# Kernel optimization log

Measured on AMD Instinct MI355X. Metric: run time of the kernel, lower is better.

The kernel has to match this reference:

```python
import jax, jax.numpy as jnp
import numpy as np
from jax import lax

B, T, V, E, H, M = 512, 60, 50000, 300, 512, 256


def _lstm_final_h(x_emb, seqlen, kernel, bias):
    """BasicLSTMCell (gate order i,j,f,o; forget_bias=1.0) with dynamic_rnn
    sequence_length semantics: state stops updating at t >= seqlen.
    x_emb: [B, T, E]; returns final h: [B, H]."""
    b = x_emb.shape[0]
    h0 = jnp.zeros((b, H), x_emb.dtype)
    c0 = jnp.zeros((b, H), x_emb.dtype)

    def step(carry, inp):
        c, h = carry
        xt, t = inp
        z = jnp.concatenate([xt, h], axis=1) @ kernel + bias  # [B, 4H]
        i, j, f, o = jnp.split(z, 4, axis=1)
        nc = c * jax.nn.sigmoid(f + 1.0) + jax.nn.sigmoid(i) * jnp.tanh(j)
        nh = jnp.tanh(nc) * jax.nn.sigmoid(o)
        valid = (t < seqlen)[:, None]
        return (jnp.where(valid, nc, c), jnp.where(valid, nh, h)), None

    (c, h), _ = lax.scan(step, (c0, h0),
                         (jnp.swapaxes(x_emb, 0, 1), jnp.arange(T)))
    return h


def setup_inputs() -> dict:
    key = jax.random.key(0)
    ks = jax.random.split(key, 8)
    return {
        "input1": jax.random.randint(ks[0], (B, T), 0, V, dtype=jnp.int32),
        "input2": jax.random.randint(ks[1], (B, T), 0, V, dtype=jnp.int32),
        "seqlen1": jax.random.randint(ks[2], (B,), 1, T + 1, dtype=jnp.int32),
        "seqlen2": jax.random.randint(ks[3], (B,), 1, T + 1, dtype=jnp.int32),
        "embeddings": jax.random.normal(ks[4], (V, E), jnp.float32) * 0.1,
        "lstm_kernel": jax.random.normal(ks[5], (E + H, 4 * H), jnp.float32) * 0.02,
        "lstm_bias": jnp.zeros((4 * H,), jnp.float32),
        "W1": jax.random.normal(ks[6], (4 * (H + 1) + 1, M), jnp.float32) * 0.02,
        "b1": jnp.zeros((1, M), jnp.float32),
        "W2": jax.random.normal(ks[7], (M, 2), jnp.float32) * 0.02,
        "b2": jnp.zeros((1, 2), jnp.float32),
    }


def reference(input1, input2, seqlen1, seqlen2, embeddings,
              lstm_kernel, lstm_bias, W1, b1, W2, b2):
    x1 = embeddings[input1]  # [B, T, E]
    x2 = embeddings[input2]
    h1 = _lstm_final_h(x1, seqlen1, lstm_kernel, lstm_bias)  # [B, H]
    h2 = _lstm_final_h(x2, seqlen2, lstm_kernel, lstm_bias)
    len1 = (seqlen1.astype(jnp.float32) / float(T))[:, None]
    len2 = (seqlen2.astype(jnp.float32) / float(T))[:, None]
    h1 = jnp.concatenate([h1, len1], axis=1)  # [B, H+1]
    h2 = jnp.concatenate([h2, len2], axis=1)
    h_sub = h1 - h2
    h_dist = jnp.sum(h_sub * h_sub, axis=1, keepdims=True)  # [B, 1]
    h_mul = h1 * h2
    h_combined = jnp.concatenate([h1, h2, h_sub, h_dist, h_mul], axis=1)
    e1 = jax.nn.relu(h_combined @ W1 + b1)  # dropout keep_prob=1 -> identity
    preds = e1 @ W2 + b2  # [B, 2]
    return preds
```

## Files before the change

### kernel.cpp

```cpp
#include <hip/hip_runtime.h>
#include <hip/hip_bf16.h>

#define BATCH 512
#define TT 60
#define EDIM 300
#define HDIM 512
#define KP1 2112
#define MDIM 256
#define V48 2400000

typedef __bf16 bf16x4 __attribute__((ext_vector_type(4)));
typedef __bf16 bf16x8 __attribute__((ext_vector_type(8)));
typedef float  f32x16 __attribute__((ext_vector_type(16)));

#define GLL16(g, l) __builtin_amdgcn_global_load_lds( \
    (const __attribute__((address_space(1))) void*)(g), \
    (__attribute__((address_space(3))) void*)(l), 16, 0, 0)

__device__ __forceinline__ float sigm(float x) {
    return 1.0f / (1.0f + __expf(-x));
}
__device__ __forceinline__ float tanh_fast(float x) {
    float e = __expf(-2.0f * fabsf(x));
    float r = (1.0f - e) / (1.0f + e);
    return x >= 0.0f ? r : -r;
}


__global__ __launch_bounds__(256) void sort_rows(const int* __restrict__ sl1,
                                                 const int* __restrict__ sl2,
                                                 int* __restrict__ rowinfo,
                                                 unsigned* __restrict__ step_done) {
    __shared__ unsigned cnt[61];
    __shared__ unsigned off[61];
    int tid = threadIdx.x;
    if (tid < 61) cnt[tid] = 0;
    if (tid >= 64 && tid < 80) step_done[tid - 64] = 0;
    __syncthreads();
    for (int i = tid; i < 1024; i += 256) {
        int sl = (i < 512) ? sl1[i] : sl2[i - 512];
        atomicAdd(&cnt[60 - sl], 1u);
    }
    __syncthreads();
    if (tid == 0) {
        unsigned s = 0;
        for (int k = 0; k < 61; ++k) { off[k] = s; s += cnt[k]; }
    }
    __syncthreads();
    for (int i = tid; i < 1024; i += 256) {
        int sc = i >= 512;
        int b = i & 511;
        int sl = sc ? sl2[b] : sl1[b];
        unsigned pos = atomicAdd(&off[60 - sl], 1u);
        rowinfo[pos] = b | (sc << 15) | (sl << 20);
    }
}

__global__ __launch_bounds__(256) void prep_w(const float* __restrict__ kern,
                                              __bf16* __restrict__ wf) {
    __shared__ float tile[64][65];
    int bk = blockIdx.x % 14;
    int bn = blockIdx.x / 14;
    int k0 = bk * 64, n0 = bn * 64;
    int tid = threadIdx.x;
#pragma unroll
    for (int i = 0; i < 16; ++i) {
        int id = i * 256 + tid;
        int kk = id >> 6, nn = id & 63;
        int kg = k0 + kk;
        int src = (kg < 300) ? kg : (kg >= 384 ? kg - 84 : -1);
        tile[kk][nn] = (src >= 0) ? kern[(size_t)src * 2048 + n0 + nn] : 0.0f;
    }
    __syncthreads();
    int gate = n0 >> 9;
    int nt = gate >> 1;
#pragma unroll
    for (int i = 0; i < 2; ++i) {
        int id = i * 256 + tid;
        int nn = id >> 3, k8 = id & 7;
        bf16x8 hv, lv;
#pragma unroll
        for (int j = 0; j < 8; ++j) {
            float v = tile[k8 * 8 + j][nn];
            __bf16 h = (__bf16)v;
            hv[j] = h;
            lv[j] = (__bf16)(v - (float)h);
        }
        int cg = (((n0 & 511) >> 4) + (nn >> 4));
        int hc = nn & 15;
        int lzc = ((gate & 1) << 4) + hc;
        int kglob = k0 + k8 * 8;
        int c = kglob >> 7;
        int j = (kglob >> 4) & 7;
        int half = k8 & 1;
        size_t o = (size_t)cg * 114688 + c * 16384 + (j * 4 + nt * 2) * 512
                 + (half * 32 + lzc) * 8;
        *(bf16x8*)(wf + o) = hv;
        *(bf16x8*)(wf + o + 512) = lv;
    }
}

__global__ __launch_bounds__(256) void prep_w1(const float* __restrict__ W1,
                                               __bf16* __restrict__ w1h,
                                               __bf16* __restrict__ w1l) {
    __shared__ float tile[64][65];
    int bk = blockIdx.x % 33;
    int bn = blockIdx.x / 33;
    int k0 = bk * 64, n0 = bn * 64;
    int tid = threadIdx.x;
#pragma unroll
    for (int i = 0; i < 16; ++i) {
        int id = i * 256 + tid;
        int kk = id >> 6, nn = id & 63;
        int kg = k0 + kk;
        tile[kk][nn] = (kg < 2053) ? W1[(size_t)kg * MDIM + n0 + nn] : 0.0f;
    }
    __syncthreads();
#pragma unroll
    for (int i = 0; i < 2; ++i) {
        int id = i * 256 + tid;
        int nn = id >> 3, k8 = (id & 7) * 8;
        bf16x8 hv, lv;
#pragma unroll
        for (int j = 0; j < 8; ++j) {
            float v = tile[k8 + j][nn];
            __bf16 h = (__bf16)v;
            hv[j] = h;
            lv[j] = (__bf16)(v - (float)h);
        }
        size_t o = (size_t)(n0 + nn) * KP1 + k0 + k8;
        *(bf16x8*)(w1h + o) = hv;
        *(bf16x8*)(w1l + o) = lv;
    }
}

__global__ __launch_bounds__(256) void prep_emb(const float* __restrict__ emb,
                                                __bf16* __restrict__ embB) {
    int id = blockIdx.x * 256 + threadIdx.x;
    if (id >= V48) return;
    int tok = id / 48;
    int k8 = id - tok * 48;
    int k0 = k8 * 8;
    float vv[8];
    const float* er = emb + (size_t)tok * EDIM + k0;
    if (k0 + 8 <= EDIM) {
        float4 f0 = *(const float4*)er;
        float4 f1 = *(const float4*)(er + 4);
        vv[0] = f0.x; vv[1] = f0.y; vv[2] = f0.z; vv[3] = f0.w;
        vv[4] = f1.x; vv[5] = f1.y; vv[6] = f1.z; vv[7] = f1.w;
    } else if (k0 < EDIM) {
        float4 f0 = *(const float4*)er;
        vv[0] = f0.x; vv[1] = f0.y; vv[2] = f0.z; vv[3] = f0.w;
        vv[4] = vv[5] = vv[6] = vv[7] = 0.f;
    } else {
#pragma unroll
        for (int j = 0; j < 8; ++j) vv[j] = 0.f;
    }
    bf16x8 hv, lv;
#pragma unroll
    for (int j = 0; j < 8; ++j) {
        __bf16 h = (__bf16)vv[j];
        hv[j] = h;
        lv[j] = (__bf16)(vv[j] - (float)h);
    }
    size_t o = (size_t)tok * 768 + k0;
    *(bf16x8*)(embB + o) = hv;
    *(bf16x8*)(embB + o + 384) = lv;
}

#define ZSTR 72

__global__ __launch_bounds__(256, 2) void lstm_all(
    const int* __restrict__ in1, const int* __restrict__ in2,
    const int* __restrict__ rowinfo,
    const __bf16* __restrict__ embB, const float* __restrict__ bias,
    const __bf16* __restrict__ wf,
    __bf16* __restrict__ XfH,
    unsigned* __restrict__ step_done,
    float* __restrict__ h_state) {

    int bx = blockIdx.x;
    int xcd = bx & 7;
    int loc = bx >> 3;
    int u = loc >> 3;
    int p = xcd & 1;
    int bt = (u < 4) ? ((u << 1) | p) : (15 - (((u - 4) << 1) | p));
    int cg = ((xcd >> 1) << 3) | (loc & 7);

    __shared__ __align__(16) __bf16 Bb[2][16384];
    __shared__ int info_s[64];

    int tid = threadIdx.x;
    int w = tid >> 6, lane = tid & 63, l31 = lane & 31;
    int s = w >> 1, kg = w & 1;

    if (tid < 64) info_s[tid] = rowinfo[bt * 64 + tid];
    __syncthreads();
    int t_end = info_s[0] >> 20;

    int rowl = s * 32 + l31;
    int inf_r = info_s[rowl];
    const int* tokptr = ((((inf_r >> 15) & 1) ? in2 : in1)) + (inf_r & 511) * TT;

    int hc16 = tid & 15;
    int hcol = (cg << 4) + hc16;
    float bi = bias[hcol], bj = bias[512 + hcol];
    float bfv = bias[1024 + hcol], bo = bias[1536 + hcol];

    float c_reg[4] = {0.f, 0.f, 0.f, 0.f};
    float h_reg[4] = {0.f, 0.f, 0.f, 0.f};

    const __bf16* wb = wf + (size_t)cg * 114688;
    auto stageB = [&](int c, int buf) {
        const __bf16* src = wb + c * 16384 + w * 4096 + lane * 8;
        __bf16* dst = &Bb[buf][w * 4096 + lane * 8];
#pragma unroll
        for (int i = 0; i < 8; ++i)
            GLL16(src + i * 512, dst + i * 512);
    };

    int ew = kg * 64 + ((lane >> 5) << 3);
    size_t hw_off = (size_t)((s * 2 + kg) * 4) * 4096 + lane * 8;

    for (int t = 0; t < t_end; ++t) {
        f32x16 acc[2];
#pragma unroll
        for (int nt = 0; nt < 2; ++nt)
#pragma unroll
            for (int r = 0; r < 16; ++r) acc[nt][r] = 0.0f;

        int tok = tokptr[t];
        const __bf16* eb = embB + (size_t)tok * 768 + ew;
        const __bf16* hrd = XfH + ((size_t)t * 16 + bt) * 65536 + hw_off;

        bf16x8 aH[4], aL[4];
        stageB(0, 0);
#pragma unroll
        for (int jj = 0; jj < 4; ++jj) {
            aH[jj] = *(const bf16x8*)(eb + jj * 16);
            aL[jj] = *(const bf16x8*)(eb + 384 + jj * 16);
        }

        if (t > 0 && tid == 0) {
            unsigned target = 32u * (unsigned)t;
            int guard = 0;
            while (__hip_atomic_load(step_done + bt, __ATOMIC_RELAXED,
                                     __HIP_MEMORY_SCOPE_AGENT) < target) {
                __builtin_amdgcn_s_sleep(2);
                if (++guard > (1 << 20)) break;
            }
        }
        __syncthreads();

#pragma unroll
        for (int c = 0; c < 7; ++c) {
            int cur = c & 1;
            bf16x8 nH[4], nL[4];
            if (c < 6) {
                stageB(c + 1, 1 - cur);
                if (c < 2) {
                    const __bf16* en = eb + (c + 1) * 128;
#pragma unroll
                    for (int jj = 0; jj < 4; ++jj) {
                        nH[jj] = *(const bf16x8*)(en + jj * 16);
                        nL[jj] = *(const bf16x8*)(en + 384 + jj * 16);
                    }
                } else {
                    const __bf16* An = hrd + (c - 2) * 4096;
#pragma unroll
                    for (int jj = 0; jj < 4; ++jj) {
                        nH[jj] = *(const bf16x8*)(An + jj * 1024);
                        nL[jj] = *(const bf16x8*)(An + jj * 1024 + 512);
                    }
                }
            }
#pragma unroll
            for (int jj = 0; jj < 4; ++jj) {
                int j = kg * 4 + jj;
#pragma unroll
                for (int nt = 0; nt < 2; ++nt) {
                    int T0 = (j * 4 + nt * 2) * 512 + lane * 8;
                    bf16x8 bh = *(const bf16x8*)(&Bb[cur][T0]);
                    bf16x8 bl = *(const bf16x8*)(&Bb[cur][T0 + 512]);
                    acc[nt] = __builtin_amdgcn_mfma_f32_32x32x16_bf16(aH[jj], bh, acc[nt], 0, 0, 0);
                    acc[nt] = __builtin_amdgcn_mfma_f32_32x32x16_bf16(aH[jj], bl, acc[nt], 0, 0, 0);
                    acc[nt] = __builtin_amdgcn_mfma_f32_32x32x16_bf16(aL[jj], bh, acc[nt], 0, 0, 0);
                }
            }
            if (c < 6) {
#pragma unroll
                for (int jj = 0; jj < 4; ++jj) { aH[jj] = nH[jj]; aL[jj] = nL[jj]; }
            }
            __syncthreads();
        }

        float* zs = (float*)&Bb[1][0];
        if (kg == 0) {
#pragma unroll
            for (int nt = 0; nt < 2; ++nt)
#pragma unroll
                for (int r = 0; r < 16; ++r) {
                    int rl = s * 32 + (r & 3) + ((r >> 2) << 3) + ((lane >> 5) << 2);
                    zs[rl * ZSTR + nt * 32 + l31] = acc[nt][r];
                }
        }
        __syncthreads();
        if (kg == 1) {
#pragma unroll
            for (int nt = 0; nt < 2; ++nt)
#pragma unroll
                for (int r = 0; r < 16; ++r) {
                    int rl = s * 32 + (r & 3) + ((r >> 2) << 3) + ((lane >> 5) << 2);
                    zs[rl * ZSTR + nt * 32 + l31] += acc[nt][r];
                }
        }
        __syncthreads();

        __bf16* zh = &Bb[0][0];
#pragma unroll
        for (int i = 0; i < 4; ++i) {
            int rl = i * 16 + (tid >> 4);
            int info = info_s[rl];
            int sl = info >> 20;
            float zi = zs[rl * ZSTR + hc16]      + bi;
            float zj = zs[rl * ZSTR + 16 + hc16] + bj;
            float zf = zs[rl * ZSTR + 32 + hc16] + bfv;
            float zo = zs[rl * ZSTR + 48 + hc16] + bo;
            float c_old = c_reg[i];
            float h_old = h_reg[i];
            float nc = c_old * sigm(zf + 1.0f) + sigm(zi) * tanh_fast(zj);
            float nh = tanh_fast(nc) * sigm(zo);
            bool valid = t < sl;
            float cs = valid ? nc : c_old;
            float hs = valid ? nh : h_old;
            c_reg[i] = cs;
            h_reg[i] = hs;
            __bf16 hh = (__bf16)hs;
            int grp = hc16 >> 3, e = hc16 & 7;
            zh[(grp * 64 + rl) * 8 + e] = hh;
            zh[((2 + grp) * 64 + rl) * 8 + e] = (__bf16)(hs - (float)hh);
        }
        __syncthreads();

        if (t + 1 < t_end) {
            int plane = tid >> 7;
            int grp = (tid >> 6) & 1;
            int rl = tid & 63;
            ulonglong2 uv = *(const ulonglong2*)(zh + ((plane * 2 + grp) * 64 + rl) * 8);
            int s2 = rl >> 5;
            size_t base = ((size_t)(t + 1) * 16 + bt) * 65536
                        + (size_t)((s2 * 2 + ((cg >> 2) & 1)) * 4 + (cg >> 3)) * 4096
                        + (cg & 3) * 1024 + plane * 512 + (grp * 32 + (rl & 31)) * 8;
            unsigned long long* dst = (unsigned long long*)(XfH + base);
            __hip_atomic_store(dst,     uv.x, __ATOMIC_RELAXED, __HIP_MEMORY_SCOPE_AGENT);
            __hip_atomic_store(dst + 1, uv.y, __ATOMIC_RELAXED, __HIP_MEMORY_SCOPE_AGENT);
        }
        __syncthreads();
        if (t + 1 < t_end && tid == 0)
            __hip_atomic_fetch_add(step_done + bt, 1u, __ATOMIC_RELAXED,
                                   __HIP_MEMORY_SCOPE_AGENT);
    }

#pragma unroll
    for (int i = 0; i < 4; ++i) {
        int rl = i * 16 + (tid >> 4);
        int info = info_s[rl];
        int b = info & 511, sc = (info >> 15) & 1;
        h_state[(size_t)((sc << 9) + b) * HDIM + hcol] = h_reg[i];
    }
}

__global__ __launch_bounds__(256) void head1(const float* __restrict__ h_state,
                                             const int* __restrict__ sl1,
                                             const int* __restrict__ sl2,
                                             __bf16* __restrict__ hch,
                                             __bf16* __restrict__ hcl) {
    int b = blockIdx.x;
    int tid = threadIdx.x;
    const float* h1 = h_state + (size_t)b * HDIM;
    const float* h2 = h_state + (size_t)(512 + b) * HDIM;
    size_t ro = (size_t)b * KP1;
    float l1 = (float)sl1[b] / (float)TT;
    float l2 = (float)sl2[b] / (float)TT;
    float part = 0.0f;
#pragma unroll
    for (int i = 0; i < 2; ++i) {
        int k = i * 256 + tid;
        float a = h1[k], c = h2[k];
        float sv = a - c;
        float mv = a * c;
        __bf16 xh;
        xh = (__bf16)a;  hch[ro + k] = xh;         hcl[ro + k] = (__bf16)(a - (float)xh);
        xh = (__bf16)c;  hch[ro + 513 + k] = xh;   hcl[ro + 513 + k] = (__bf16)(c - (float)xh);
        xh = (__bf16)sv; hch[ro + 1026 + k] = xh;  hcl[ro + 1026 + k] = (__bf16)(sv - (float)xh);
        xh = (__bf16)mv; hch[ro + 1540 + k] = xh;  hcl[ro + 1540 + k] = (__bf16)(mv - (float)xh);
        part += sv * sv;
    }
    __shared__ float red[4];
#pragma unroll
    for (int off = 32; off > 0; off >>= 1) part += __shfl_down(part, off, 64);
    if ((tid & 63) == 0) red[tid >> 6] = part;
    __syncthreads();
    if (tid == 0) {
        float d = red[0] + red[1] + red[2] + red[3];
        float ls = l1 - l2;
        d += ls * ls;
        float vals[5] = {l1, l2, ls, d, l1 * l2};
        int pos[5] = {512, 1025, 1538, 1539, 2052};
#pragma unroll
        for (int i = 0; i < 5; ++i) {
            __bf16 xh = (__bf16)vals[i];
            hch[ro + pos[i]] = xh;
            hcl[ro + pos[i]] = (__bf16)(vals[i] - (float)xh);
        }
    }
}

__global__ __launch_bounds__(512, 2) void head2m(
    const __bf16* __restrict__ hch, const __bf16* __restrict__ hcl,
    const __bf16* __restrict__ w1h, const __bf16* __restrict__ w1l,
    float* __restrict__ part) {

    __shared__ __align__(16) __bf16 Bb[2][64 * 512];

    int tid = threadIdx.x;
    int bx = blockIdx.x;
    int mt = bx >> 3;
    int n2 = (bx >> 2) & 1;
    int ks = bx & 3;
    int w = tid >> 6, lane = tid & 63, l31 = lane & 31;
    int half8 = (lane >> 5) << 3;
    int s = w >> 1, nh = w & 1;
    int kbase = ks * 528;

    int k8 = tid & 15;
    int jb = k8 >> 1;
    int rb = (tid >> 4) & 31;
    size_t gboff[8];
    int lo[8];
#pragma unroll
    for (int i = 0; i < 8; ++i) {
        int r = ((i & 3) << 5) + rb;
        int plane = i >> 2;
        int ng = n2 * 128 + r;
        gboff[i] = (size_t)ng * KP1 + k8 * 8;
        int nt = r >> 5;
        int colp = ((r & 31) + (jb << 2)) & 31;
        lo[i] = ((((jb << 2) + nt) << 1) + plane) * 512 + (colp + ((k8 & 1) << 5)) * 8;
    }

    const __bf16* Ah0 = hch + (size_t)(mt * 128 + s * 32 + l31) * KP1 + kbase + half8;
    const __bf16* Al0 = hcl + (size_t)(mt * 128 + s * 32 + l31) * KP1 + kbase + half8;

    bf16x8 rB[8];
    f32x16 acc[2];
#pragma unroll
    for (int nt = 0; nt < 2; ++nt)
#pragma unroll
        for (int r = 0; r < 16; ++r) acc[nt][r] = 0.0f;

#pragma unroll
    for (int i = 0; i < 8; ++i)
        rB[i] = *(const bf16x8*)(((i >= 4) ? w1l : w1h) + gboff[i] + kbase);
#pragma unroll
    for (int i = 0; i < 8; ++i) *(bf16x8*)(&Bb[0][lo[i]]) = rB[i];
    __syncthreads();

    for (int c = 0; c < 5; ++c) {
        int cur = c & 1;
        if (c < 4) {
            int k0 = kbase + (c + 1) * 128;
            bool tail = (c + 1 == 4);
#pragma unroll
            for (int i = 0; i < 8; ++i) {
                if (!tail || k8 < 2)
                    rB[i] = *(const bf16x8*)(((i >= 4) ? w1l : w1h) + gboff[i] + k0);
            }
        }
        int jmax = (c == 4) ? 1 : 8;
        for (int j = 0; j < jmax; ++j) {
            bf16x8 ah = *(const bf16x8*)(Ah0 + c * 128 + j * 16);
            bf16x8 al = *(const bf16x8*)(Al0 + c * 128 + j * 16);
            int cp = ((l31 + (j << 2)) & 31) + ((lane >> 5) << 5);
#pragma unroll
            for (int ntl = 0; ntl < 2; ++ntl) {
                int ntg = nh * 2 + ntl;
                const __bf16* bp = &Bb[cur][(((j << 2) + ntg) << 1) * 512 + cp * 8];
                bf16x8 bh = *(const bf16x8*)bp;
                bf16x8 bl = *(const bf16x8*)(bp + 512);
                acc[ntl] = __builtin_amdgcn_mfma_f32_32x32x16_bf16(ah, bh, acc[ntl], 0, 0, 0);
                acc[ntl] = __builtin_amdgcn_mfma_f32_32x32x16_bf16(ah, bl, acc[ntl], 0, 0, 0);
                acc[ntl] = __builtin_amdgcn_mfma_f32_32x32x16_bf16(al, bh, acc[ntl], 0, 0, 0);
            }
        }
        if (c < 4) {
#pragma unroll
            for (int i = 0; i < 8; ++i) *(bf16x8*)(&Bb[1 - cur][lo[i]]) = rB[i];
        }
        __syncthreads();
    }

#pragma unroll
    for (int ntl = 0; ntl < 2; ++ntl)
#pragma unroll
        for (int r = 0; r < 16; ++r) {
            int row = mt * 128 + s * 32 + (r & 3) + ((r >> 2) << 3) + ((lane >> 5) << 2);
            int col = n2 * 128 + nh * 64 + ntl * 32 + l31;
            part[((size_t)ks * 512 + row) * MDIM + col] = acc[ntl][r];
        }
}

__global__ __launch_bounds__(256) void head3(const float* __restrict__ part,
                                             const float* __restrict__ b1,
                                             const float* __restrict__ W2,
                                             const float* __restrict__ b2,
                                             float* __restrict__ out) {
    int row = blockIdx.x;
    int tid = threadIdx.x;
    float sv = b1[tid];
#pragma unroll
    for (int ks = 0; ks < 4; ++ks)
        sv += part[((size_t)ks * 512 + row) * MDIM + tid];
    float e = fmaxf(sv, 0.0f);
    float p0 = e * W2[tid * 2 + 0];
    float p1 = e * W2[tid * 2 + 1];
#pragma unroll
    for (int off = 32; off > 0; off >>= 1) {
        p0 += __shfl_down(p0, off, 64);
        p1 += __shfl_down(p1, off, 64);
    }
    __shared__ float r0[4], r1[4];
    if ((tid & 63) == 0) { r0[tid >> 6] = p0; r1[tid >> 6] = p1; }
    __syncthreads();
    if (tid == 0) out[row * 2 + 0] = r0[0] + r0[1] + r0[2] + r0[3] + b2[0];
    if (tid == 1) out[row * 2 + 1] = r1[0] + r1[1] + r1[2] + r1[3] + b2[1];
}

extern "C" void kernel_launch(void* const* d_in, const int* in_sizes, int n_in,
                              void* d_out, int out_size, void* d_ws, size_t ws_size,
                              hipStream_t stream) {
    const int*   in1  = (const int*)d_in[0];
    const int*   in2  = (const int*)d_in[1];
    const int*   sl1  = (const int*)d_in[2];
    const int*   sl2  = (const int*)d_in[3];
    const float* emb  = (const float*)d_in[4];
    const float* kern = (const float*)d_in[5];
    const float* bias = (const float*)d_in[6];
    const float* W1   = (const float*)d_in[7];
    const float* b1   = (const float*)d_in[8];
    const float* W2   = (const float*)d_in[9];
    const float* b2   = (const float*)d_in[10];
    float* out = (float*)d_out;

    char* ws = (char*)d_ws;
    int*      rowinfo   = (int*)ws;
    unsigned* step_done = (unsigned*)(ws + 4096u);
    float*  h_state = (float*)(ws + 2097152u);
    __bf16* wf   = (__bf16*)(ws + 6291456u);
    __bf16* hch  = (__bf16*)(ws + 13631488u);
    __bf16* hcl  = (__bf16*)(ws + 15794176u);
    __bf16* w1h  = (__bf16*)(ws + 17956864u);
    __bf16* w1l  = (__bf16*)(ws + 19038208u);
    float*  part = (float*)(ws + 20119552u);
    __bf16* embB = (__bf16*)(ws + 23068672u);
    __bf16* XfH  = (__bf16*)(ws + 100663296u);

    hipMemsetAsync(ws + 13631488u, 0, 4325376u, stream);
    hipMemsetAsync(ws + 100663296u, 0, 2097152u, stream);

    sort_rows<<<dim3(1), dim3(256), 0, stream>>>(sl1, sl2, rowinfo, step_done);
    prep_w<<<dim3(14 * 32), dim3(256), 0, stream>>>(kern, wf);
    prep_w1<<<dim3(33 * 4), dim3(256), 0, stream>>>(W1, w1h, w1l);
    prep_emb<<<dim3(9375), dim3(256), 0, stream>>>(emb, embB);

    lstm_all<<<dim3(512), dim3(256), 0, stream>>>(
        in1, in2, rowinfo, embB, bias, wf, XfH, step_done, h_state);

    head1<<<dim3(512), dim3(256), 0, stream>>>(h_state, sl1, sl2, hch, hcl);
    head2m<<<dim3(32), dim3(512), 0, stream>>>(hch, hcl, w1h, w1l, part);
    head3<<<dim3(512), dim3(256), 0, stream>>>(part, b1, W2, b2, out);
}
```

Measured before the change: 1.273 ms.

## Load LSTM weight fragments directly into registers and defer step barrier

Replaces the double-buffered LDS staging of weight tiles (global_load_lds plus a per-chunk __syncthreads) with direct global-to-register loads of each wave's B fragments. The cross-block step wait moves to chunk 2, so the embedding-input chunks run before the dependency on the previous step's h. The two k-group partial sums go to separate LDS buffers and are added during the gate computation, which removes one barrier and one read-modify-write pass. The aim is fewer barriers and less LDS traffic per timestep. In exchange it adds register pressure and relies on global/L2 latency for the weights with no LDS staging.

Result: slower. 2.102 ms (+65.1%).

```diff
diff --git a/kernel.cpp b/kernel.cpp
--- a/kernel.cpp
+++ b/kernel.cpp
@@ -12,10 +12,6 @@
 typedef __bf16 bf16x4 __attribute__((ext_vector_type(4)));
 typedef __bf16 bf16x8 __attribute__((ext_vector_type(8)));
 typedef float  f32x16 __attribute__((ext_vector_type(16)));
-
-#define GLL16(g, l) __builtin_amdgcn_global_load_lds( \
-    (const __attribute__((address_space(1))) void*)(g), \
-    (__attribute__((address_space(3))) void*)(l), 16, 0, 0)
 
 __device__ __forceinline__ float sigm(float x) {
     return 1.0f / (1.0f + __expf(-x));
@@ -168,7 +164,7 @@
     *(bf16x8*)(embB + o + 384) = lv;
 }
 
-#define ZSTR 72
+#define ZSTR 68
 
 __global__ __launch_bounds__(256, 2) void lstm_all(
     const int* __restrict__ in1, const int* __restrict__ in2,
@@ -187,7 +183,8 @@
     int bt = (u < 4) ? ((u << 1) | p) : (15 - (((u - 4) << 1) | p));
     int cg = ((xcd >> 1) << 3) | (loc & 7);
 
-    __shared__ __align__(16) __bf16 Bb[2][16384];
+    __shared__ float zs[2][64 * ZSTR];
+    __shared__ __align__(16) __bf16 zh[2 * 2 * 64 * 8];
     __shared__ int info_s[64];
 
     int tid = threadIdx.x;
@@ -210,14 +207,7 @@
     float c_reg[4] = {0.f, 0.f, 0.f, 0.f};
     float h_reg[4] = {0.f, 0.f, 0.f, 0.f};
 
-    const __bf16* wb = wf + (size_t)cg * 114688;
-    auto stageB = [&](int c, int buf) {
-        const __bf16* src = wb + c * 16384 + w * 4096 + lane * 8;
-        __bf16* dst = &Bb[buf][w * 4096 + lane * 8];
-#pragma unroll
-        for (int i = 0; i < 8; ++i)
-            GLL16(src + i * 512, dst + i * 512);
-    };
+    const __bf16* wbl = wf + (size_t)cg * 114688 + (size_t)kg * 8192 + lane * 8;
 
     int ew = kg * 64 + ((lane >> 5) << 3);
     size_t hw_off = (size_t)((s * 2 + kg) * 4) * 4096 + lane * 8;
@@ -234,30 +224,39 @@
         const __bf16* hrd = XfH + ((size_t)t * 16 + bt) * 65536 + hw_off;
 
         bf16x8 aH[4], aL[4];
-        stageB(0, 0);
 #pragma unroll
         for (int jj = 0; jj < 4; ++jj) {
             aH[jj] = *(const bf16x8*)(eb + jj * 16);
             aL[jj] = *(const bf16x8*)(eb + 384 + jj * 16);
         }
 
-        if (t > 0 && tid == 0) {
-            unsigned target = 32u * (unsigned)t;
-            int guard = 0;
-            while (__hip_atomic_load(step_done + bt, __ATOMIC_RELAXED,
-                                     __HIP_MEMORY_SCOPE_AGENT) < target) {
-                __builtin_amdgcn_s_sleep(2);
-                if (++guard > (1 << 20)) break;
+#pragma unroll
+        for (int c = 0; c < 7; ++c) {
+            const __bf16* bc = wbl + c * 16384;
+            bf16x8 bH[4][2], bL[4][2];
+#pragma unroll
+            for (int jj = 0; jj < 4; ++jj)
+#pragma unroll
+                for (int nt = 0; nt < 2; ++nt) {
+                    bH[jj][nt] = *(const bf16x8*)(bc + jj * 2048 + nt * 1024);
+                    bL[jj][nt] = *(const bf16x8*)(bc + jj * 2048 + nt * 1024 + 512);
+                }
+
+            if (c == 2 && t > 0) {
+                if (tid == 0) {
+                    unsigned target = 32u * (unsigned)t;
+                    int guard = 0;
+                    while (__hip_atomic_load(step_done + bt, __ATOMIC_RELAXED,
+                                             __HIP_MEMORY_SCOPE_AGENT) < target) {
+                        __builtin_amdgcn_s_sleep(1);
+                        if (++guard > (1 << 20)) break;
+                    }
+                }
+                __syncthreads();
             }
-        }
-        __syncthreads();
-
-#pragma unroll
-        for (int c = 0; c < 7; ++c) {
-            int cur = c & 1;
+
             bf16x8 nH[4], nL[4];
             if (c < 6) {
-                stageB(c + 1, 1 - cur);
                 if (c < 2) {
                     const __bf16* en = eb + (c + 1) * 128;
 #pragma unroll
@@ -274,58 +273,39 @@
                     }
                 }
             }
-#pragma unroll
-            for (int jj = 0; jj < 4; ++jj) {
-                int j = kg * 4 + jj;
+
+#pragma unroll
+            for (int jj = 0; jj < 4; ++jj)
 #pragma unroll
                 for (int nt = 0; nt < 2; ++nt) {
-                    int T0 = (j * 4 + nt * 2) * 512 + lane * 8;
-                    bf16x8 bh = *(const bf16x8*)(&Bb[cur][T0]);
-                    bf16x8 bl = *(const bf16x8*)(&Bb[cur][T0 + 512]);
-                    acc[nt] = __builtin_amdgcn_mfma_f32_32x32x16_bf16(aH[jj], bh, acc[nt], 0, 0, 0);
-                    acc[nt] = __builtin_amdgcn_mfma_f32_32x32x16_bf16(aH[jj], bl, acc[nt], 0, 0, 0);
-                    acc[nt] = __builtin_amdgcn_mfma_f32_32x32x16_bf16(aL[jj], bh, acc[nt], 0, 0, 0);
+                    acc[nt] = __builtin_amdgcn_mfma_f32_32x32x16_bf16(aH[jj], bH[jj][nt], acc[nt], 0, 0, 0);
+                    acc[nt] = __builtin_amdgcn_mfma_f32_32x32x16_bf16(aH[jj], bL[jj][nt], acc[nt], 0, 0, 0);
+                    acc[nt] = __builtin_amdgcn_mfma_f32_32x32x16_bf16(aL[jj], bH[jj][nt], acc[nt], 0, 0, 0);
                 }
-            }
             if (c < 6) {
 #pragma unroll
                 for (int jj = 0; jj < 4; ++jj) { aH[jj] = nH[jj]; aL[jj] = nL[jj]; }
             }
-            __syncthreads();
-        }
-
-        float* zs = (float*)&Bb[1][0];
-        if (kg == 0) {
-#pragma unroll
-            for (int nt = 0; nt < 2; ++nt)
-#pragma unroll
-                for (int r = 0; r < 16; ++r) {
-                    int rl = s * 32 + (r & 3) + ((r >> 2) << 3) + ((lane >> 5) << 2);
-                    zs[rl * ZSTR + nt * 32 + l31] = acc[nt][r];
-                }
-        }
+        }
+
+#pragma unroll
+        for (int nt = 0; nt < 2; ++nt)
+#pragma unroll
+            for (int r = 0; r < 16; ++r) {
+                int rl = s * 32 + (r & 3) + ((r >> 2) << 3) + ((lane >> 5) << 2);
+                zs[kg][rl * ZSTR + nt * 32 + l31] = acc[nt][r];
+            }
         __syncthreads();
-        if (kg == 1) {
-#pragma unroll
-            for (int nt = 0; nt < 2; ++nt)
-#pragma unroll
-                for (int r = 0; r < 16; ++r) {
-                    int rl = s * 32 + (r & 3) + ((r >> 2) << 3) + ((lane >> 5) << 2);
-                    zs[rl * ZSTR + nt * 32 + l31] += acc[nt][r];
-                }
-        }
-        __syncthreads();
-
-        __bf16* zh = &Bb[0][0];
+
 #pragma unroll
         for (int i = 0; i < 4; ++i) {
             int rl = i * 16 + (tid >> 4);
             int info = info_s[rl];
             int sl = info >> 20;
-            float zi = zs[rl * ZSTR + hc16]      + bi;
-            float zj = zs[rl * ZSTR + 16 + hc16] + bj;
-            float zf = zs[rl * ZSTR + 32 + hc16] + bfv;
-            float zo = zs[rl * ZSTR + 48 + hc16] + bo;
+            float zi = zs[0][rl * ZSTR + hc16]      + zs[1][rl * ZSTR + hc16]      + bi;
+            float zj = zs[0][rl * ZSTR + 16 + hc16] + zs[1][rl * ZSTR + 16 + hc16] + bj;
+            float zf = zs[0][rl * ZSTR + 32 + hc16] + zs[1][rl * ZSTR + 32 + hc16] + bfv;
+            float zo = zs[0][rl * ZSTR + 48 + hc16] + zs[1][rl * ZSTR + 48 + hc16] + bo;
             float c_old = c_reg[i];
             float h_old = h_reg[i];
             float nc = c_old * sigm(zf + 1.0f) + sigm(zi) * tanh_fast(zj);
```

## Software-pipeline LSTM recurrence: prefetch next step, defer spin-wait, fuse partial-sum reduction

Applied to the files above, without the earlier changes.

Restructures the persistent LSTM step loop. Weight staging and embedding loads for the next timestep are issued before the current step signals completion. The cross-block spin-wait is moved to just before the first chunk that needs h, so the x-part of the GEMM runs while other blocks finish. The two K-group partial sums now go to separate LDS regions and are added during the gate math, which removes a serialized read-modify-write pass. Full __syncthreads are replaced by raw s_barrier with hand-written waitcnt and sched_barrier fences. The manual vmcnt/lgkmcnt counts risk memory-ordering bugs if the number of loads in flight changes.

Measured after the change: 1.233 ms. 3.2% less time.

```diff
diff --git a/kernel.cpp b/kernel.cpp
--- a/kernel.cpp
+++ b/kernel.cpp
@@ -16,6 +16,9 @@
 #define GLL16(g, l) __builtin_amdgcn_global_load_lds( \
     (const __attribute__((address_space(1))) void*)(g), \
     (__attribute__((address_space(3))) void*)(l), 16, 0, 0)
+
+#define SBAR()  __builtin_amdgcn_s_barrier()
+#define SCHED0() __builtin_amdgcn_sched_barrier(0)
 
 __device__ __forceinline__ float sigm(float x) {
     return 1.0f / (1.0f + __expf(-x));
@@ -188,6 +191,7 @@
     int cg = ((xcd >> 1) << 3) | (loc & 7);
 
     __shared__ __align__(16) __bf16 Bb[2][16384];
+    __shared__ __align__(16) __bf16 zh[2048];
     __shared__ int info_s[64];
 
     int tid = threadIdx.x;
@@ -222,6 +226,18 @@
     int ew = kg * 64 + ((lane >> 5) << 3);
     size_t hw_off = (size_t)((s * 2 + kg) * 4) * 4096 + lane * 8;
 
+    int tok = tokptr[0];
+    stageB(0, 0);
+    SCHED0();
+    bf16x8 aH[4], aL[4];
+    const __bf16* eb = embB + (size_t)tok * 768 + ew;
+#pragma unroll
+    for (int jj = 0; jj < 4; ++jj) {
+        aH[jj] = *(const bf16x8*)(eb + jj * 16);
+        aL[jj] = *(const bf16x8*)(eb + 384 + jj * 16);
+    }
+    SCHED0();
+
     for (int t = 0; t < t_end; ++t) {
         f32x16 acc[2];
 #pragma unroll
@@ -229,35 +245,31 @@
 #pragma unroll
             for (int r = 0; r < 16; ++r) acc[nt][r] = 0.0f;
 
-        int tok = tokptr[t];
-        const __bf16* eb = embB + (size_t)tok * 768 + ew;
         const __bf16* hrd = XfH + ((size_t)t * 16 + bt) * 65536 + hw_off;
 
-        bf16x8 aH[4], aL[4];
-        stageB(0, 0);
-#pragma unroll
-        for (int jj = 0; jj < 4; ++jj) {
-            aH[jj] = *(const bf16x8*)(eb + jj * 16);
-            aL[jj] = *(const bf16x8*)(eb + 384 + jj * 16);
-        }
-
-        if (t > 0 && tid == 0) {
-            unsigned target = 32u * (unsigned)t;
-            int guard = 0;
-            while (__hip_atomic_load(step_done + bt, __ATOMIC_RELAXED,
-                                     __HIP_MEMORY_SCOPE_AGENT) < target) {
-                __builtin_amdgcn_s_sleep(2);
-                if (++guard > (1 << 20)) break;
-            }
-        }
-        __syncthreads();
-
 #pragma unroll
         for (int c = 0; c < 7; ++c) {
-            int cur = c & 1;
+            int cur = (t + c) & 1;
+            asm volatile("s_waitcnt vmcnt(8)" ::: "memory");
+            SBAR();
+            SCHED0();
+            if (c == 2 && t > 0) {
+                if (tid == 0) {
+                    unsigned target = 32u * (unsigned)t;
+                    int guard = 0;
+                    while (__hip_atomic_load(step_done + bt, __ATOMIC_RELAXED,
+                                             __HIP_MEMORY_SCOPE_AGENT) < target) {
+                        __builtin_amdgcn_s_sleep(1);
+                        if (++guard > (1 << 20)) break;
+                    }
+                }
+                SBAR();
+                SCHED0();
+            }
             bf16x8 nH[4], nL[4];
             if (c < 6) {
                 stageB(c + 1, 1 - cur);
+                SCHED0();
                 if (c < 2) {
                     const __bf16* en = eb + (c + 1) * 128;
 #pragma unroll
@@ -273,6 +285,7 @@
                         nL[jj] = *(const bf16x8*)(An + jj * 1024 + 512);
                     }
                 }
+                SCHED0();
             }
 #pragma unroll
             for (int jj = 0; jj < 4; ++jj) {
@@ -291,41 +304,36 @@
 #pragma unroll
                 for (int jj = 0; jj < 4; ++jj) { aH[jj] = nH[jj]; aL[jj] = nL[jj]; }
             }
-            __syncthreads();
-        }
-
-        float* zs = (float*)&Bb[1][0];
-        if (kg == 0) {
-#pragma unroll
-            for (int nt = 0; nt < 2; ++nt)
-#pragma unroll
-                for (int r = 0; r < 16; ++r) {
-                    int rl = s * 32 + (r & 3) + ((r >> 2) << 3) + ((lane >> 5) << 2);
-                    zs[rl * ZSTR + nt * 32 + l31] = acc[nt][r];
-                }
-        }
-        __syncthreads();
-        if (kg == 1) {
-#pragma unroll
-            for (int nt = 0; nt < 2; ++nt)
-#pragma unroll
-                for (int r = 0; r < 16; ++r) {
-                    int rl = s * 32 + (r & 3) + ((r >> 2) << 3) + ((lane >> 5) << 2);
-                    zs[rl * ZSTR + nt * 32 + l31] += acc[nt][r];
-                }
-        }
-        __syncthreads();
-
-        __bf16* zh = &Bb[0][0];
+        }
+
+        SBAR();
+        SCHED0();
+
+        int tn = (t + 1 < TT) ? t + 1 : TT - 1;
+        int tok_n = tokptr[tn];
+        SCHED0();
+
+        float* zsb = (float*)&Bb[0][0];
+#pragma unroll
+        for (int nt = 0; nt < 2; ++nt)
+#pragma unroll
+            for (int r = 0; r < 16; ++r) {
+                int rl = s * 32 + (r & 3) + ((r >> 2) << 3) + ((lane >> 5) << 2);
+                zsb[kg * 4608 + rl * ZSTR + nt * 32 + l31] = acc[nt][r];
+            }
+        asm volatile("s_waitcnt lgkmcnt(0)" ::: "memory");
+        SBAR();
+        SCHED0();
+
 #pragma unroll
         for (int i = 0; i < 4; ++i) {
             int rl = i * 16 + (tid >> 4);
             int info = info_s[rl];
             int sl = info >> 20;
-            float zi = zs[rl * ZSTR + hc16]      + bi;
-            float zj = zs[rl * ZSTR + 16 + hc16] + bj;
-            float zf = zs[rl * ZSTR + 32 + hc16] + bfv;
-            float zo = zs[rl * ZSTR + 48 + hc16] + bo;
+            float zi = zsb[rl * ZSTR + hc16]      + zsb[4608 + rl * ZSTR + hc16]      + bi;
+            float zj = zsb[rl * ZSTR + 16 + hc16] + zsb[4608 + rl * ZSTR + 16 + hc16] + bj;
+            float zf = zsb[rl * ZSTR + 32 + hc16] + zsb[4608 + rl * ZSTR + 32 + hc16] + bfv;
+            float zo = zsb[rl * ZSTR + 48 + hc16] + zsb[4608 + rl * ZSTR + 48 + hc16] + bo;
             float c_old = c_reg[i];
             float h_old = h_reg[i];
             float nc = c_old * sigm(zf + 1.0f) + sigm(zi) * tanh_fast(zj);
@@ -340,7 +348,9 @@
             zh[(grp * 64 + rl) * 8 + e] = hh;
             zh[((2 + grp) * 64 + rl) * 8 + e] = (__bf16)(hs - (float)hh);
         }
-        __syncthreads();
+        asm volatile("s_waitcnt lgkmcnt(0)" ::: "memory");
+        SBAR();
+        SCHED0();
 
         if (t + 1 < t_end) {
             int plane = tid >> 7;
@@ -354,11 +364,22 @@
             unsigned long long* dst = (unsigned long long*)(XfH + base);
             __hip_atomic_store(dst,     uv.x, __ATOMIC_RELAXED, __HIP_MEMORY_SCOPE_AGENT);
             __hip_atomic_store(dst + 1, uv.y, __ATOMIC_RELAXED, __HIP_MEMORY_SCOPE_AGENT);
-        }
-        __syncthreads();
-        if (t + 1 < t_end && tid == 0)
-            __hip_atomic_fetch_add(step_done + bt, 1u, __ATOMIC_RELAXED,
-                                   __HIP_MEMORY_SCOPE_AGENT);
+            SCHED0();
+            stageB(0, (t + 1) & 1);
+            SCHED0();
+            eb = embB + (size_t)tok_n * 768 + ew;
+#pragma unroll
+            for (int jj = 0; jj < 4; ++jj) {
+                aH[jj] = *(const bf16x8*)(eb + jj * 16);
+                aL[jj] = *(const bf16x8*)(eb + 384 + jj * 16);
+            }
+            SCHED0();
+            asm volatile("s_waitcnt vmcnt(16)" ::: "memory");
+            SBAR();
+            if (tid == 0)
+                __hip_atomic_fetch_add(step_done + bt, 1u, __ATOMIC_RELAXED,
+                                       __HIP_MEMORY_SCOPE_AGENT);
+        }
     }
 
 #pragma unroll
```
